# Kernel optimization log

Hardware: AMD Instinct MI355X
Metric: run time of the kernel (lower is better)

Reference implementation:

```python
import jax, jax.numpy as jnp
import numpy as np

B, TE, TD, HE, HD = 16, 512, 64, 512, 512


def setup_inputs() -> dict:
    key = jax.random.key(0)
    k1, k2, k3, k4, k5 = jax.random.split(key, 5)
    return {
        "encoder_out_seq": jax.random.normal(k1, (B, TE, HE), dtype=jnp.float32),
        "decoder_out_seq": jax.random.normal(k2, (B, TD, HD), dtype=jnp.float32),
        "W_a": jax.random.normal(k3, (HE, HE), dtype=jnp.float32) * 0.05,
        "U_a": jax.random.normal(k4, (HD, HE), dtype=jnp.float32) * 0.05,
        "V_a": jax.random.normal(k5, (HE, 1), dtype=jnp.float32) * 0.05,
    }


def reference(encoder_out_seq, decoder_out_seq, W_a, U_a, V_a):
    # Bahdanau additive attention, batched over all decoder steps at once
    # (the original K.rnn loop over Td is embarrassingly parallel).
    Ws = jnp.einsum('bte,eh->bth', encoder_out_seq, W_a)   # [B,Te,He]
    Uh = jnp.einsum('bdk,kh->bdh', decoder_out_seq, U_a)   # [B,Td,He]
    # additive combine + tanh: [B,Td,Te,He]
    act = jnp.tanh(Ws[:, None, :, :] + Uh[:, :, None, :])
    e = jnp.einsum('bdth,h->bdt', act, V_a[:, 0])          # [B,Td,Te]
    e = jax.nn.softmax(e, axis=-1)                          # attention weights
    c = jnp.einsum('bdt,bth->bdh', e, encoder_out_seq)      # [B,Td,He] context
    return (c, e)
```

## Files before the change

### kernel.cpp

```cpp
#include <hip/hip_runtime.h>
#include <hip/hip_bf16.h>

#define BB 16
#define TE 512
#define TD 64
#define HE 512

#define PRESCALE 2.8853900817779268f

typedef __attribute__((ext_vector_type(8))) short bf16x8;
typedef __attribute__((ext_vector_type(4))) float f32x4;

__device__ __forceinline__ float fexp2(float x) {
#if __has_builtin(__builtin_amdgcn_exp2f)
    return __builtin_amdgcn_exp2f(x);
#else
    return exp2f(x);
#endif
}
__device__ __forceinline__ float frcp(float x) {
#if __has_builtin(__builtin_amdgcn_rcpf)
    return __builtin_amdgcn_rcpf(x);
#else
    return __fdividef(1.f, x);
#endif
}

__device__ __forceinline__ void split2(float x, unsigned short& h, unsigned short& l) {
    __hip_bfloat16 hb = __float2bfloat16(x);
    h = *(unsigned short*)&hb;
    float r = x - __bfloat162float(hb);
    __hip_bfloat16 lb = __float2bfloat16(r);
    l = *(unsigned short*)&lb;
}

__device__ __forceinline__ void gload16(const unsigned short* g, void* l) {
    __builtin_amdgcn_global_load_lds(
        (const __attribute__((address_space(1))) unsigned int*)g,
        (__attribute__((address_space(3))) unsigned int*)l, 16, 0, 0);
}


__global__ __launch_bounds__(256)
void split_enc_k8(const float* __restrict__ X,
                  unsigned short* __restrict__ Ah, unsigned short* __restrict__ Al,
                  unsigned short* __restrict__ Th, unsigned short* __restrict__ Tl)
{
    __shared__ float t[32][33];
    const int tid = threadIdx.x;
    const int r0 = blockIdx.y * 32, c0 = blockIdx.x * 32;
    const int b  = blockIdx.z;
    const size_t bo = (size_t)b * TE * HE;
    const int i = tid >> 3, j4 = (tid & 7) * 4;

    const float4 v = *(const float4*)&X[bo + (size_t)(r0 + i) * HE + c0 + j4];

    ushort4 h, l;
    split2(v.x, h.x, l.x); split2(v.y, h.y, l.y);
    split2(v.z, h.z, l.z); split2(v.w, h.w, l.w);
    {
        const int m = b * TE + r0 + i;
        const int k = c0 + j4;
        const size_t o = ((size_t)(k >> 3) * (BB * TE) + m) * 8 + (k & 7);
        *(ushort4*)&Ah[o] = h;
        *(ushort4*)&Al[o] = l;
    }

    t[i][j4 + 0] = v.x; t[i][j4 + 1] = v.y; t[i][j4 + 2] = v.z; t[i][j4 + 3] = v.w;
    __syncthreads();

    split2(t[j4 + 0][i], h.x, l.x);
    split2(t[j4 + 1][i], h.y, l.y);
    split2(t[j4 + 2][i], h.z, l.z);
    split2(t[j4 + 3][i], h.w, l.w);
    {
        const int k = r0 + j4;
        const size_t o = bo + ((size_t)(k >> 3) * HE + c0 + i) * 8 + (k & 7);
        *(ushort4*)&Th[o] = h;
        *(ushort4*)&Tl[o] = l;
    }
}

__global__ __launch_bounds__(256)
void split_misc_k8(const float* __restrict__ dec,
                   unsigned short* __restrict__ dH, unsigned short* __restrict__ dL,
                   const float* __restrict__ Wa,
                   unsigned short* __restrict__ wH, unsigned short* __restrict__ wL,
                   const float* __restrict__ Ua,
                   unsigned short* __restrict__ uH, unsigned short* __restrict__ uL)
{
    const int tid = threadIdx.x;
    const int i = tid >> 3, j4 = (tid & 7) * 4;
    const int z = blockIdx.z;

    if (z == 2) {
        const int r0 = blockIdx.y * 32, c0 = blockIdx.x * 32;
        const int M = BB * TD;
        const float4 v = *(const float4*)&dec[(size_t)(r0 + i) * HE + c0 + j4];
        ushort4 h, l;
        split2(v.x, h.x, l.x); split2(v.y, h.y, l.y);
        split2(v.z, h.z, l.z); split2(v.w, h.w, l.w);
        const int m = r0 + i, k = c0 + j4;
        const size_t o = ((size_t)(k >> 3) * M + m) * 8 + (k & 7);
        *(ushort4*)&dH[o] = h;
        *(ushort4*)&dL[o] = l;
        return;
    }

    if (blockIdx.y >= 16) return;
    __shared__ float t[32][33];
    const float* X = z ? Ua : Wa;
    unsigned short* H = z ? uH : wH;
    unsigned short* L = z ? uL : wL;
    const int r0 = blockIdx.y * 32, c0 = blockIdx.x * 32;

    const float4 v = *(const float4*)&X[(size_t)(r0 + i) * HE + c0 + j4];
    t[i][j4 + 0] = v.x; t[i][j4 + 1] = v.y; t[i][j4 + 2] = v.z; t[i][j4 + 3] = v.w;
    __syncthreads();

    ushort4 h, l;
    split2(t[j4 + 0][i], h.x, l.x);
    split2(t[j4 + 1][i], h.y, l.y);
    split2(t[j4 + 2][i], h.z, l.z);
    split2(t[j4 + 3][i], h.w, l.w);
    const int r = r0 + j4;
    const size_t o = ((size_t)(r >> 3) * HE + c0 + i) * 8 + (r & 7);
    *(ushort4*)&H[o] = h;
    *(ushort4*)&L[o] = l;
}

__global__ __launch_bounds__(256)
void gemm_ws_uh(const unsigned short* __restrict__ eAh, const unsigned short* __restrict__ eAl,
                const unsigned short* __restrict__ wBh, const unsigned short* __restrict__ wBl,
                float* __restrict__ Ew,
                const unsigned short* __restrict__ dAh, const unsigned short* __restrict__ dAl,
                const unsigned short* __restrict__ uBh, const unsigned short* __restrict__ uBl,
                float* __restrict__ Eu)
{
    __shared__ char smem[2][32768];

    const int tid  = threadIdx.x;
    const int lane = tid & 63;
    const int wave = tid >> 6;
    const int wr = wave >> 1, wc = wave & 1;
    const int fr = lane & 15, fg = lane >> 4;

    const unsigned short *Ahi, *Alo, *Bhi, *Blo;
    float* C;
    int M, row0;
    if (blockIdx.y < 64) {
        Ahi = eAh; Alo = eAl; Bhi = wBh; Blo = wBl; C = Ew;
        M = BB * TE; row0 = blockIdx.y * 128;
    } else {
        Ahi = dAh; Alo = dAl; Bhi = uBh; Blo = uBl; C = Eu;
        M = BB * TD; row0 = (blockIdx.y - 64) * 128;
    }
    const int N = HE, K = HE;
    const int col0 = blockIdx.x * 128;

    f32x4 acc[4][4];
#pragma unroll
    for (int mi = 0; mi < 4; ++mi)
#pragma unroll
        for (int ni = 0; ni < 4; ++ni)
            acc[mi][ni] = (f32x4){0.f, 0.f, 0.f, 0.f};

    auto STAGE = [&](int buf, int k0) {
#pragma unroll
        for (int c = 0; c < 2; ++c) {
            const int bi  = (c * 4 + wave) * 64 + lane;
            const int g   = bi >> 7;
            const int idx = bi & 127;
            int mrow = row0 + idx; if (mrow >= M) mrow -= M;
            const int ncol = col0 + idx;
            const size_t ao = ((size_t)((k0 >> 3) + g) * M + mrow) * 8;
            const size_t bo = ((size_t)((k0 >> 3) + g) * N + ncol) * 8;
            const int lb = (c * 4 + wave) * 1024;
            gload16(Ahi + ao, smem[buf] + lb);
            gload16(Alo + ao, smem[buf] + 8192 + lb);
            gload16(Bhi + bo, smem[buf] + 16384 + lb);
            gload16(Blo + bo, smem[buf] + 24576 + lb);
        }
    };

    STAGE(0, 0);
    __syncthreads();

    int buf = 0;
    for (int k0 = 0; k0 < K; k0 += 32) {
        if (k0 + 32 < K) STAGE(buf ^ 1, k0 + 32);

        const int gb = fg << 7;
        bf16x8 ah[4], al[4], bh[4], bl[4];
#pragma unroll
        for (int mi = 0; mi < 4; ++mi) {
            const int off = (gb + wr * 64 + mi * 16 + fr) * 16;
            ah[mi] = *(const bf16x8*)(smem[buf] + off);
            al[mi] = *(const bf16x8*)(smem[buf] + 8192 + off);
        }
#pragma unroll
        for (int ni = 0; ni < 4; ++ni) {
            const int off = (gb + wc * 64 + ni * 16 + fr) * 16;
            bh[ni] = *(const bf16x8*)(smem[buf] + 16384 + off);
            bl[ni] = *(const bf16x8*)(smem[buf] + 24576 + off);
        }
#pragma unroll
        for (int mi = 0; mi < 4; ++mi)
#pragma unroll
            for (int ni = 0; ni < 4; ++ni) {
                acc[mi][ni] = __builtin_amdgcn_mfma_f32_16x16x32_bf16(ah[mi], bh[ni], acc[mi][ni], 0, 0, 0);
                acc[mi][ni] = __builtin_amdgcn_mfma_f32_16x16x32_bf16(ah[mi], bl[ni], acc[mi][ni], 0, 0, 0);
                acc[mi][ni] = __builtin_amdgcn_mfma_f32_16x16x32_bf16(al[mi], bh[ni], acc[mi][ni], 0, 0, 0);
            }
        __syncthreads();
        buf ^= 1;
    }

#pragma unroll
    for (int mi = 0; mi < 4; ++mi) {
        const int rbase = row0 + wr * 64 + mi * 16 + fg * 4;
#pragma unroll
        for (int ni = 0; ni < 4; ++ni) {
            const int col = col0 + wc * 64 + ni * 16 + fr;
#pragma unroll
            for (int r = 0; r < 4; ++r) {
                const int row = rbase + r;
                if (row < M) C[(size_t)row * N + col] = fexp2(acc[mi][ni][r] * PRESCALE);
            }
        }
    }
}

__global__ __launch_bounds__(256)
void gemm_mfma3(const unsigned short* __restrict__ Ahi, const unsigned short* __restrict__ Alo,
                const unsigned short* __restrict__ Bhi, const unsigned short* __restrict__ Blo,
                float* __restrict__ C, int M, int N, int K,
                long long sA, long long sB, long long sC)
{
    __shared__ char smem[2][32768];

    const int tid  = threadIdx.x;
    const int lane = tid & 63;
    const int wave = tid >> 6;
    const int wr = wave >> 1, wc = wave & 1;
    const int fr = lane & 15, fg = lane >> 4;
    const int row0 = blockIdx.y * 128;
    const int col0 = blockIdx.x * 128;

    Ahi += (size_t)blockIdx.z * sA; Alo += (size_t)blockIdx.z * sA;
    Bhi += (size_t)blockIdx.z * sB; Blo += (size_t)blockIdx.z * sB;
    C   += (size_t)blockIdx.z * sC;

    f32x4 acc[4][4];
#pragma unroll
    for (int mi = 0; mi < 4; ++mi)
#pragma unroll
        for (int ni = 0; ni < 4; ++ni)
            acc[mi][ni] = (f32x4){0.f, 0.f, 0.f, 0.f};

    auto STAGE = [&](int buf, int k0) {
#pragma unroll
        for (int c = 0; c < 2; ++c) {
            const int bi  = (c * 4 + wave) * 64 + lane;
            const int g   = bi >> 7;
            const int idx = bi & 127;
            int mrow = row0 + idx; if (mrow >= M) mrow -= M;
            const int ncol = col0 + idx;
            const size_t ao = ((size_t)((k0 >> 3) + g) * M + mrow) * 8;
            const size_t bo = ((size_t)((k0 >> 3) + g) * N + ncol) * 8;
            const int lb = (c * 4 + wave) * 1024;
            gload16(Ahi + ao, smem[buf] + lb);
            gload16(Alo + ao, smem[buf] + 8192 + lb);
            gload16(Bhi + bo, smem[buf] + 16384 + lb);
            gload16(Blo + bo, smem[buf] + 24576 + lb);
        }
    };

    STAGE(0, 0);
    __syncthreads();

    int buf = 0;
    for (int k0 = 0; k0 < K; k0 += 32) {
        if (k0 + 32 < K) STAGE(buf ^ 1, k0 + 32);

        const int gb = fg << 7;
        bf16x8 ah[4], al[4], bh[4], bl[4];
#pragma unroll
        for (int mi = 0; mi < 4; ++mi) {
            const int off = (gb + wr * 64 + mi * 16 + fr) * 16;
            ah[mi] = *(const bf16x8*)(smem[buf] + off);
            al[mi] = *(const bf16x8*)(smem[buf] + 8192 + off);
        }
#pragma unroll
        for (int ni = 0; ni < 4; ++ni) {
            const int off = (gb + wc * 64 + ni * 16 + fr) * 16;
            bh[ni] = *(const bf16x8*)(smem[buf] + 16384 + off);
            bl[ni] = *(const bf16x8*)(smem[buf] + 24576 + off);
        }
#pragma unroll
        for (int mi = 0; mi < 4; ++mi)
#pragma unroll
            for (int ni = 0; ni < 4; ++ni) {
                acc[mi][ni] = __builtin_amdgcn_mfma_f32_16x16x32_bf16(ah[mi], bh[ni], acc[mi][ni], 0, 0, 0);
                acc[mi][ni] = __builtin_amdgcn_mfma_f32_16x16x32_bf16(ah[mi], bl[ni], acc[mi][ni], 0, 0, 0);
                acc[mi][ni] = __builtin_amdgcn_mfma_f32_16x16x32_bf16(al[mi], bh[ni], acc[mi][ni], 0, 0, 0);
            }
        __syncthreads();
        buf ^= 1;
    }

#pragma unroll
    for (int mi = 0; mi < 4; ++mi) {
        const int rbase = row0 + wr * 64 + mi * 16 + fg * 4;
#pragma unroll
        for (int ni = 0; ni < 4; ++ni) {
            const int col = col0 + wc * 64 + ni * 16 + fr;
#pragma unroll
            for (int r = 0; r < 4; ++r) {
                const int row = rbase + r;
                if (row < M) C[(size_t)row * N + col] = acc[mi][ni][r];
            }
        }
    }
}

__global__ __launch_bounds__(256)
void gemm_f32(const float* __restrict__ A, const float* __restrict__ Bm,
              float* __restrict__ C, int M, int N, int K,
              long long sAb, long long sBb, long long sCb, float scale, int emode)
{
    __shared__ float As[16][68];
    __shared__ float Bs[16][68];

    const int tid = threadIdx.x;
    const int tx  = tid & 15;
    const int ty  = tid >> 4;
    const int row0 = blockIdx.y * 64;
    const int col0 = blockIdx.x * 64;

    A  += (long long)blockIdx.z * sAb;
    Bm += (long long)blockIdx.z * sBb;
    C  += (long long)blockIdx.z * sCb;

    float acc[4][4] = {};

    for (int k0 = 0; k0 < K; k0 += 16) {
        {
            const int r = tid >> 2;
            const int c = (tid & 3) * 4;
            const float4 av = *(const float4*)&A[(long long)(row0 + r) * K + k0 + c];
            As[c + 0][r] = av.x; As[c + 1][r] = av.y;
            As[c + 2][r] = av.z; As[c + 3][r] = av.w;
        }
        {
            const int r = tid >> 4;
            const int c = (tid & 15) * 4;
            *(float4*)&Bs[r][c] = *(const float4*)&Bm[(long long)(k0 + r) * N + col0 + c];
        }
        __syncthreads();

#pragma unroll
        for (int kk = 0; kk < 16; ++kk) {
            const float4 a = *(const float4*)&As[kk][ty * 4];
            const float4 b = *(const float4*)&Bs[kk][tx * 4];
            acc[0][0] += a.x * b.x; acc[0][1] += a.x * b.y; acc[0][2] += a.x * b.z; acc[0][3] += a.x * b.w;
            acc[1][0] += a.y * b.x; acc[1][1] += a.y * b.y; acc[1][2] += a.y * b.z; acc[1][3] += a.y * b.w;
            acc[2][0] += a.z * b.x; acc[2][1] += a.z * b.y; acc[2][2] += a.z * b.z; acc[2][3] += a.z * b.w;
            acc[3][0] += a.w * b.x; acc[3][1] += a.w * b.y; acc[3][2] += a.w * b.z; acc[3][3] += a.w * b.w;
        }
        __syncthreads();
    }

#pragma unroll
    for (int i = 0; i < 4; ++i) {
        float4 o;
        o.x = acc[i][0] * scale; o.y = acc[i][1] * scale;
        o.z = acc[i][2] * scale; o.w = acc[i][3] * scale;
        if (emode) { o.x = fexp2(o.x); o.y = fexp2(o.y); o.z = fexp2(o.z); o.w = fexp2(o.w); }
        *(float4*)&C[(long long)(row0 + ty * 4 + i) * N + col0 + tx * 4] = o;
    }
}

__global__ __launch_bounds__(256)
void scores_raw(const float* __restrict__ Ew, const float* __restrict__ Eu,
                const float* __restrict__ V, float* __restrict__ part)
{
    __shared__ float Ws_s[32][64];
    __shared__ float Uh_s[32][64];
    __shared__ float Vr_s[HE];

    const int tid = threadIdx.x;
    const int tg  = tid & 7;
    const int dg  = tid >> 3;

    const int tt0  = blockIdx.x * 32;
    const int quar = blockIdx.y & 3;
    const int d0   = (blockIdx.y >> 2) * 32;
    const int b    = blockIdx.z;

    const float* Wsg = Ew + (long long)b * TE * HE;
    const float* Uhg = Eu + ((long long)b * TD + d0) * HE;

    if (tid < 128) {
        const float4 v = *(const float4*)&V[tid * 4];
        float4 o; o.x = -2.f * v.x; o.y = -2.f * v.y; o.z = -2.f * v.z; o.w = -2.f * v.w;
        *(float4*)&Vr_s[tid * 4] = o;
    }

    float acc[4] = {0.f, 0.f, 0.f, 0.f};
    const int wswz = tg & 7;
    const int uswz = dg & 7;
    const int hbase = quar * (HE / 4);

    for (int hc = hbase; hc < hbase + HE / 4; hc += 64) {
        __syncthreads();
#pragma unroll
        for (int k = 0; k < 2; ++k) {
            const int idx = tid + k * 256;
            const int r   = idx >> 4;
            const int c4  = idx & 15;
            const float4 wv = *(const float4*)&Wsg[(long long)(tt0 + r) * HE + hc + c4 * 4];
            *(float4*)&Ws_s[r][(c4 ^ ((r >> 2) & 7)) * 4] = wv;
            const float4 uv = *(const float4*)&Uhg[(long long)r * HE + hc + c4 * 4];
            *(float4*)&Uh_s[r][(c4 ^ (r & 7)) * 4] = uv;
        }
        __syncthreads();

#pragma unroll 4
        for (int hs = 0; hs < 64; hs += 4) {
            const int h4 = hs >> 2;
            const float4 vv = *(const float4*)&Vr_s[hc + hs];
            const float4 u  = *(const float4*)&Uh_s[dg][(h4 ^ uswz) * 4];
#pragma unroll
            for (int i = 0; i < 4; ++i) {
                const float4 w = *(const float4*)&Ws_s[tg * 4 + i][(h4 ^ wswz) * 4];
                acc[i] = fmaf(vv.x, frcp(fmaf(w.x, u.x, 1.f)), acc[i]);
                acc[i] = fmaf(vv.y, frcp(fmaf(w.y, u.y, 1.f)), acc[i]);
                acc[i] = fmaf(vv.z, frcp(fmaf(w.z, u.z, 1.f)), acc[i]);
                acc[i] = fmaf(vv.w, frcp(fmaf(w.w, u.w, 1.f)), acc[i]);
            }
        }
    }

    float* dst = part + (size_t)quar * (BB * TD * TE);
    float4 o; o.x = acc[0]; o.y = acc[1]; o.z = acc[2]; o.w = acc[3];
    *(float4*)&dst[((long long)b * TD + d0 + dg) * TE + tt0 + tg * 4] = o;
}

__global__ __launch_bounds__(256)
void softmax_rows(const float* __restrict__ part, float* __restrict__ e,
                  unsigned short* __restrict__ H, unsigned short* __restrict__ L)
{
    const int lane = threadIdx.x & 63;
    const int wave = threadIdx.x >> 6;
    const long long row = blockIdx.x * 4 + wave;

    float4 a = {0.f, 0.f, 0.f, 0.f}, c = {0.f, 0.f, 0.f, 0.f};
#pragma unroll
    for (int q = 0; q < 4; ++q) {
        const float* p = part + (size_t)q * (BB * TD * TE) + row * TE;
        const float4 aq = *(const float4*)&p[lane * 4];
        const float4 cq = *(const float4*)&p[lane * 4 + 256];
        a.x += aq.x; a.y += aq.y; a.z += aq.z; a.w += aq.w;
        c.x += cq.x; c.y += cq.y; c.z += cq.z; c.w += cq.w;
    }

    float m = fmaxf(fmaxf(fmaxf(a.x, a.y), fmaxf(a.z, a.w)),
                    fmaxf(fmaxf(c.x, c.y), fmaxf(c.z, c.w)));
#pragma unroll
    for (int off = 32; off; off >>= 1) m = fmaxf(m, __shfl_xor(m, off));

    a.x = __expf(a.x - m); a.y = __expf(a.y - m); a.z = __expf(a.z - m); a.w = __expf(a.w - m);
    c.x = __expf(c.x - m); c.y = __expf(c.y - m); c.z = __expf(c.z - m); c.w = __expf(c.w - m);

    float s = (a.x + a.y + a.z + a.w) + (c.x + c.y + c.z + c.w);
#pragma unroll
    for (int off = 32; off; off >>= 1) s += __shfl_xor(s, off);

    const float inv = __fdividef(1.f, s);
    a.x *= inv; a.y *= inv; a.z *= inv; a.w *= inv;
    c.x *= inv; c.y *= inv; c.z *= inv; c.w *= inv;
    float* pe = e + row * TE;
    *(float4*)&pe[lane * 4] = a;
    *(float4*)&pe[lane * 4 + 256] = c;

    if (H) {
        const int b = (int)(row >> 6);
        const int d = (int)(row & 63);
        const size_t base = (size_t)b * (TD * TE);
        ushort4 h, l;
        {
            const int t0 = lane * 4;
            const size_t o = base + ((size_t)(t0 >> 3) * TD + d) * 8 + (t0 & 7);
            split2(a.x, h.x, l.x); split2(a.y, h.y, l.y);
            split2(a.z, h.z, l.z); split2(a.w, h.w, l.w);
            *(ushort4*)&H[o] = h;
            *(ushort4*)&L[o] = l;
        }
        {
            const int t0 = lane * 4 + 256;
            const size_t o = base + ((size_t)(t0 >> 3) * TD + d) * 8 + (t0 & 7);
            split2(c.x, h.x, l.x); split2(c.y, h.y, l.y);
            split2(c.z, h.z, l.z); split2(c.w, h.w, l.w);
            *(ushort4*)&H[o] = h;
            *(ushort4*)&L[o] = l;
        }
    }
}

extern "C" void kernel_launch(void* const* d_in, const int* in_sizes, int n_in,
                              void* d_out, int out_size, void* d_ws, size_t ws_size,
                              hipStream_t stream)
{
    const float* enc = (const float*)d_in[0];
    const float* dec = (const float*)d_in[1];
    const float* Wa  = (const float*)d_in[2];
    const float* Ua  = (const float*)d_in[3];
    const float* Va  = (const float*)d_in[4];

    float* out   = (float*)d_out;
    float* c_out = out;
    float* e_out = out + (size_t)BB * TD * HE;

    char* w = (char*)d_ws;
    float* Ew  = (float*)(w);
    float* Eu  = (float*)(w + 16777216);
    unsigned short* encAh = (unsigned short*)(w + 18874368);
    unsigned short* encAl = (unsigned short*)(w + 27262976);
    unsigned short* encTh = (unsigned short*)(w + 35651584);
    unsigned short* encTl = (unsigned short*)(w + 44040192);
    unsigned short* decAh = (unsigned short*)(w + 52428800);
    unsigned short* decAl = (unsigned short*)(w + 53477376);
    unsigned short* WaTh  = (unsigned short*)(w + 54525952);
    unsigned short* WaTl  = (unsigned short*)(w + 55050240);
    unsigned short* UaTh  = (unsigned short*)(w + 55574528);
    unsigned short* UaTl  = (unsigned short*)(w + 56098816);
    unsigned short* eh    = (unsigned short*)(w + 56623104);
    unsigned short* el    = (unsigned short*)(w + 57671680);
    float* part = (float*)(w + 58720256);
    const size_t REQUIRED = 67108864;

    dim3 blk(256);

    if (ws_size >= REQUIRED) {
        split_enc_k8<<<dim3(16, 16, BB), blk, 0, stream>>>(enc, encAh, encAl, encTh, encTl);
        split_misc_k8<<<dim3(16, 32, 3), blk, 0, stream>>>(
            dec, decAh, decAl, Wa, WaTh, WaTl, Ua, UaTh, UaTl);

        gemm_ws_uh<<<dim3(4, 72, 1), blk, 0, stream>>>(
            encAh, encAl, WaTh, WaTl, Ew, decAh, decAl, UaTh, UaTl, Eu);

        scores_raw<<<dim3(TE / 32, (TD / 32) * 4, BB), blk, 0, stream>>>(Ew, Eu, Va, part);
        softmax_rows<<<dim3(BB * TD / 4), blk, 0, stream>>>(part, e_out, eh, el);

        gemm_mfma3<<<dim3(4, 1, BB), blk, 0, stream>>>(
            eh, el, encTh, encTl, c_out, TD, HE, TE,
            (long long)TD * TE, (long long)TE * HE, (long long)TD * HE);
    } else {
        float* pf = (float*)(w + 18874368);
        gemm_f32<<<dim3(HE / 64, (BB * TE) / 64, 1), blk, 0, stream>>>(
            enc, Wa, Ew, BB * TE, HE, HE, 0, 0, 0, PRESCALE, 1);
        gemm_f32<<<dim3(HE / 64, (BB * TD) / 64, 1), blk, 0, stream>>>(
            dec, Ua, Eu, BB * TD, HE, HE, 0, 0, 0, PRESCALE, 1);
        scores_raw<<<dim3(TE / 32, (TD / 32) * 4, BB), blk, 0, stream>>>(Ew, Eu, Va, pf);
        softmax_rows<<<dim3(BB * TD / 4), blk, 0, stream>>>(pf, e_out, nullptr, nullptr);
        gemm_f32<<<dim3(HE / 64, TD / 64, BB), blk, 0, stream>>>(
            e_out, enc, c_out, TD, HE, TE,
            (long long)TD * TE, (long long)TE * HE, (long long)TD * HE, 1.0f, 0);
    }
}
```

Measured before the change: 92.12 us.

## Use 64x64 swizzled tiles for bf16 splits and relax GEMM pipeline barriers

```diff
diff --git a/kernel.cpp b/kernel.cpp
--- a/kernel.cpp
+++ b/kernel.cpp
@@ -41,44 +41,82 @@
 }
 
 
+
+__device__ __forceinline__ void tile_load(const float* __restrict__ src, int ld,
+                                          float (*tile)[64], int tid)
+{
+#pragma unroll
+    for (int p = 0; p < 4; ++p) {
+        const int f = p * 256 + tid;
+        const int r = f >> 4, c4 = f & 15;
+        const float4 v = *(const float4*)&src[(size_t)r * ld + c4 * 4];
+        *(float4*)&tile[r][((c4 ^ (r & 7))) << 2] = v;
+    }
+}
+
+__device__ __forceinline__ void tile_outA(float (*tile)[64],
+                                          unsigned short* __restrict__ H,
+                                          unsigned short* __restrict__ L,
+                                          size_t Ms, size_t sg_base, size_t m_base, int tid)
+{
+#pragma unroll
+    for (int p = 0; p < 2; ++p) {
+        const int task = p * 256 + tid;
+        const int s = task >> 6, mm = task & 63;
+        const float4 x = *(const float4*)&tile[mm][(((s << 1)    ) ^ (mm & 7)) << 2];
+        const float4 y = *(const float4*)&tile[mm][(((s << 1) | 1) ^ (mm & 7)) << 2];
+        ushort4 ha, la, hb, lb;
+        split2(x.x, ha.x, la.x); split2(x.y, ha.y, la.y);
+        split2(x.z, ha.z, la.z); split2(x.w, ha.w, la.w);
+        split2(y.x, hb.x, lb.x); split2(y.y, hb.y, lb.y);
+        split2(y.z, hb.z, lb.z); split2(y.w, hb.w, lb.w);
+        const size_t o = ((sg_base + s) * Ms + m_base + mm) * 8;
+        *(ushort4*)&H[o] = ha; *(ushort4*)&H[o + 4] = hb;
+        *(ushort4*)&L[o] = la; *(ushort4*)&L[o + 4] = lb;
+    }
+}
+
+__device__ __forceinline__ void tile_outT(float (*tile)[64],
+                                          unsigned short* __restrict__ H,
+                                          unsigned short* __restrict__ L,
+                                          size_t Ns, size_t sg_base, size_t n_base, int tid)
+{
+#pragma unroll
+    for (int p = 0; p < 2; ++p) {
+        const int task = p * 256 + tid;
+        const int s2 = task >> 6, hh = task & 63;
+        float v[8];
+#pragma unroll
+        for (int q = 0; q < 8; ++q) {
+            const int r = s2 * 8 + q;
+            v[q] = tile[r][((((hh >> 2)) ^ (r & 7)) << 2) + (hh & 3)];
+        }
+        ushort4 ha, la, hb, lb;
+        split2(v[0], ha.x, la.x); split2(v[1], ha.y, la.y);
+        split2(v[2], ha.z, la.z); split2(v[3], ha.w, la.w);
+        split2(v[4], hb.x, lb.x); split2(v[5], hb.y, lb.y);
+        split2(v[6], hb.z, lb.z); split2(v[7], hb.w, lb.w);
+        const size_t o = ((sg_base + s2) * Ns + n_base + hh) * 8;
+        *(ushort4*)&H[o] = ha; *(ushort4*)&H[o + 4] = hb;
+        *(ushort4*)&L[o] = la; *(ushort4*)&L[o + 4] = lb;
+    }
+}
+
 __global__ __launch_bounds__(256)
 void split_enc_k8(const float* __restrict__ X,
                   unsigned short* __restrict__ Ah, unsigned short* __restrict__ Al,
                   unsigned short* __restrict__ Th, unsigned short* __restrict__ Tl)
 {
-    __shared__ float t[32][33];
+    __shared__ float tile[64][64];
     const int tid = threadIdx.x;
-    const int r0 = blockIdx.y * 32, c0 = blockIdx.x * 32;
-    const int b  = blockIdx.z;
+    const int h0 = blockIdx.x * 64, t0 = blockIdx.y * 64, b = blockIdx.z;
     const size_t bo = (size_t)b * TE * HE;
-    const int i = tid >> 3, j4 = (tid & 7) * 4;
-
-    const float4 v = *(const float4*)&X[bo + (size_t)(r0 + i) * HE + c0 + j4];
-
-    ushort4 h, l;
-    split2(v.x, h.x, l.x); split2(v.y, h.y, l.y);
-    split2(v.z, h.z, l.z); split2(v.w, h.w, l.w);
-    {
-        const int m = b * TE + r0 + i;
-        const int k = c0 + j4;
-        const size_t o = ((size_t)(k >> 3) * (BB * TE) + m) * 8 + (k & 7);
-        *(ushort4*)&Ah[o] = h;
-        *(ushort4*)&Al[o] = l;
-    }
-
-    t[i][j4 + 0] = v.x; t[i][j4 + 1] = v.y; t[i][j4 + 2] = v.z; t[i][j4 + 3] = v.w;
+
+    tile_load(X + bo + (size_t)t0 * HE + h0, HE, tile, tid);
     __syncthreads();
 
-    split2(t[j4 + 0][i], h.x, l.x);
-    split2(t[j4 + 1][i], h.y, l.y);
-    split2(t[j4 + 2][i], h.z, l.z);
-    split2(t[j4 + 3][i], h.w, l.w);
-    {
-        const int k = r0 + j4;
-        const size_t o = bo + ((size_t)(k >> 3) * HE + c0 + i) * 8 + (k & 7);
-        *(ushort4*)&Th[o] = h;
-        *(ushort4*)&Tl[o] = l;
-    }
+    tile_outA(tile, Ah, Al, (size_t)BB * TE, h0 >> 3, (size_t)b * TE + t0, tid);
+    tile_outT(tile, Th + bo, Tl + bo, HE, t0 >> 3, h0, tid);
 }
 
 __global__ __launch_bounds__(256)
@@ -89,44 +127,25 @@
                    const float* __restrict__ Ua,
                    unsigned short* __restrict__ uH, unsigned short* __restrict__ uL)
 {
+    __shared__ float tile[64][64];
     const int tid = threadIdx.x;
-    const int i = tid >> 3, j4 = (tid & 7) * 4;
     const int z = blockIdx.z;
 
     if (z == 2) {
-        const int r0 = blockIdx.y * 32, c0 = blockIdx.x * 32;
-        const int M = BB * TD;
-        const float4 v = *(const float4*)&dec[(size_t)(r0 + i) * HE + c0 + j4];
-        ushort4 h, l;
-        split2(v.x, h.x, l.x); split2(v.y, h.y, l.y);
-        split2(v.z, h.z, l.z); split2(v.w, h.w, l.w);
-        const int m = r0 + i, k = c0 + j4;
-        const size_t o = ((size_t)(k >> 3) * M + m) * 8 + (k & 7);
-        *(ushort4*)&dH[o] = h;
-        *(ushort4*)&dL[o] = l;
+        const int m0 = blockIdx.y * 64, h0 = blockIdx.x * 64;
+        tile_load(dec + (size_t)m0 * HE + h0, HE, tile, tid);
+        __syncthreads();
+        tile_outA(tile, dH, dL, (size_t)BB * TD, h0 >> 3, m0, tid);
         return;
     }
-
-    if (blockIdx.y >= 16) return;
-    __shared__ float t[32][33];
+    if (blockIdx.y >= 8) return;
     const float* X = z ? Ua : Wa;
     unsigned short* H = z ? uH : wH;
     unsigned short* L = z ? uL : wL;
-    const int r0 = blockIdx.y * 32, c0 = blockIdx.x * 32;
-
-    const float4 v = *(const float4*)&X[(size_t)(r0 + i) * HE + c0 + j4];
-    t[i][j4 + 0] = v.x; t[i][j4 + 1] = v.y; t[i][j4 + 2] = v.z; t[i][j4 + 3] = v.w;
+    const int r0 = blockIdx.y * 64, c0 = blockIdx.x * 64;
+    tile_load(X + (size_t)r0 * HE + c0, HE, tile, tid);
     __syncthreads();
-
-    ushort4 h, l;
-    split2(t[j4 + 0][i], h.x, l.x);
-    split2(t[j4 + 1][i], h.y, l.y);
-    split2(t[j4 + 2][i], h.z, l.z);
-    split2(t[j4 + 3][i], h.w, l.w);
-    const int r = r0 + j4;
-    const size_t o = ((size_t)(r >> 3) * HE + c0 + i) * 8 + (r & 7);
-    *(ushort4*)&H[o] = h;
-    *(ushort4*)&L[o] = l;
+    tile_outT(tile, H, L, HE, r0 >> 3, c0, tid);
 }
 
 __global__ __launch_bounds__(256)
@@ -184,11 +203,15 @@
     };
 
     STAGE(0, 0);
-    __syncthreads();
 
     int buf = 0;
     for (int k0 = 0; k0 < K; k0 += 32) {
-        if (k0 + 32 < K) STAGE(buf ^ 1, k0 + 32);
+        if (k0 + 32 < K) {
+            STAGE(buf ^ 1, k0 + 32);
+            asm volatile("s_waitcnt vmcnt(8)\n\ts_barrier" ::: "memory");
+        } else {
+            asm volatile("s_waitcnt vmcnt(0)\n\ts_barrier" ::: "memory");
+        }
 
         const int gb = fg << 7;
         bf16x8 ah[4], al[4], bh[4], bl[4];
@@ -212,7 +235,7 @@
                 acc[mi][ni] = __builtin_amdgcn_mfma_f32_16x16x32_bf16(ah[mi], bl[ni], acc[mi][ni], 0, 0, 0);
                 acc[mi][ni] = __builtin_amdgcn_mfma_f32_16x16x32_bf16(al[mi], bh[ni], acc[mi][ni], 0, 0, 0);
             }
-        __syncthreads();
+        asm volatile("s_barrier" ::: "memory");
         buf ^= 1;
     }
 
@@ -277,11 +300,15 @@
     };
 
     STAGE(0, 0);
-    __syncthreads();
 
     int buf = 0;
     for (int k0 = 0; k0 < K; k0 += 32) {
-        if (k0 + 32 < K) STAGE(buf ^ 1, k0 + 32);
+        if (k0 + 32 < K) {
+            STAGE(buf ^ 1, k0 + 32);
+            asm volatile("s_waitcnt vmcnt(8)\n\ts_barrier" ::: "memory");
+        } else {
+            asm volatile("s_waitcnt vmcnt(0)\n\ts_barrier" ::: "memory");
+        }
 
         const int gb = fg << 7;
         bf16x8 ah[4], al[4], bh[4], bl[4];
@@ -305,7 +332,7 @@
                 acc[mi][ni] = __builtin_amdgcn_mfma_f32_16x16x32_bf16(ah[mi], bl[ni], acc[mi][ni], 0, 0, 0);
                 acc[mi][ni] = __builtin_amdgcn_mfma_f32_16x16x32_bf16(al[mi], bh[ni], acc[mi][ni], 0, 0, 0);
             }
-        __syncthreads();
+        asm volatile("s_barrier" ::: "memory");
         buf ^= 1;
     }
 
@@ -543,8 +570,9 @@
     dim3 blk(256);
 
     if (ws_size >= REQUIRED) {
-        split_enc_k8<<<dim3(16, 16, BB), blk, 0, stream>>>(enc, encAh, encAl, encTh, encTl);
-        split_misc_k8<<<dim3(16, 32, 3), blk, 0, stream>>>(
+        split_enc_k8<<<dim3(HE / 64, TE / 64, BB), blk, 0, stream>>>(
+            enc, encAh, encAl, encTh, encTl);
+        split_misc_k8<<<dim3(8, 16, 3), blk, 0, stream>>>(
             dec, decAh, decAl, Wa, WaTh, WaTl, Ua, UaTh, UaTl);
 
         gemm_ws_uh<<<dim3(4, 72, 1), blk, 0, stream>>>(
```

Result: no change. 90.70 us (-1.5%).
